# Optimization experiments

Measured on AMD Instinct MI355X. Metric: run time of the kernel, lower is better.

## Reference

```python
import jax, jax.numpy as jnp
import numpy as np

NUM_EMBEDDINGS = 1024
EMBEDDING_DIM = 128
COMMITMENT_COST = 1.0
DECAY = 0.99
EPSILON = 1e-05
N_TOKENS = 65536


def setup_inputs() -> dict:
    key = jax.random.key(0)
    k1, k2, k3 = jax.random.split(key, 3)
    inputs = jax.random.normal(k1, (N_TOKENS, EMBEDDING_DIM), dtype=jnp.float32)
    embedding = jax.random.normal(k2, (NUM_EMBEDDINGS, EMBEDDING_DIM), dtype=jnp.float32) * 0.01
    cluster_size = jnp.ones((NUM_EMBEDDINGS,), dtype=jnp.float32)
    embed_avg = jax.random.normal(k3, (NUM_EMBEDDINGS, EMBEDDING_DIM), dtype=jnp.float32) * 0.01
    return {"inputs": inputs, "embedding": embedding,
            "cluster_size": cluster_size, "embed_avg": embed_avg}


def reference(inputs, embedding, cluster_size, embed_avg):
    # inputs: [N, D], embedding: [K, D]
    flat = inputs.reshape(-1, EMBEDDING_DIM)
    distances = (jnp.sum(flat * flat, axis=1, keepdims=True)
                 + jnp.sum(embedding * embedding, axis=1)
                 - 2.0 * flat @ embedding.T)
    idx = jnp.argmin(distances, axis=1)                       # [N]
    quantized = embedding[idx].reshape(inputs.shape)          # direct gather (same math as one-hot matmul)

    # EMA update (training path); one-hot matmuls replaced by bincount/segment_sum
    dw = jnp.zeros((NUM_EMBEDDINGS,), dtype=flat.dtype).at[idx].add(1.0)   # encodings.sum(0)
    new_cluster_size = cluster_size * DECAY + (1.0 - DECAY) * dw
    dw_embed = jax.ops.segment_sum(flat, idx, num_segments=NUM_EMBEDDINGS)  # encodings.T @ flat
    new_embed_avg = embed_avg * DECAY + (1.0 - DECAY) * dw_embed
    n = jnp.sum(new_cluster_size)
    cs = (new_cluster_size + EPSILON) / (n + NUM_EMBEDDINGS * EPSILON) * n
    new_embedding = new_embed_avg / cs[:, None]

    # losses (quantized/inputs detach semantics are identical values in fwd)
    diff2 = jnp.mean((quantized - inputs) ** 2)
    loss = diff2 + COMMITMENT_COST * diff2

    # straight-through estimator: value equals quantized
    quantized_st = inputs + jax.lax.stop_gradient(quantized - inputs)
    return (quantized_st, loss, idx, new_embedding, new_cluster_size, new_embed_avg)
```

## Files before the change

kernel.cpp:

```cpp
#include <hip/hip_runtime.h>

typedef __attribute__((ext_vector_type(8))) _Float16 half8;
typedef __attribute__((ext_vector_type(4))) float f32x4;

constexpr int NTOK = 65536;
constexpr int DIM  = 128;
constexpr int NK   = 1024;

__global__ void bprep_k(const float* __restrict__ emb, char* __restrict__ bp,
                        float* __restrict__ embT, float* __restrict__ e2s,
                        double* __restrict__ en2d, int* __restrict__ nflag) {
  int i = blockIdx.x * 256 + threadIdx.x;
  if (i == 0) *nflag = 0;
  int c = i >> 4;
  int g = i & 15;
  float4 v0 = *(const float4*)&emb[c * 128 + g * 8];
  float4 v1 = *(const float4*)&emb[c * 128 + g * 8 + 4];
  float vf[8] = {v0.x, v0.y, v0.z, v0.w, v1.x, v1.y, v1.z, v1.w};
  half8 hv;
  double pacc = 0.0;
#pragma unroll
  for (int j = 0; j < 8; j++) {
    hv[j] = (_Float16)vf[j];
    embT[(g * 8 + j) * NK + c] = vf[j];
    pacc = fma((double)vf[j], (double)vf[j], pacc);
  }
  int chunk = c >> 5, n = (c >> 4) & 1, cl = c & 15;
  int kk = g >> 2, lo4 = g & 3;
  *(half8*)(bp + chunk * 8192 + kk * 2048 + n * 1024 + (lo4 * 16 + cl) * 16) = hv;
#pragma unroll
  for (int mask = 1; mask < 16; mask <<= 1) pacc += __shfl_xor(pacc, mask);
  if (g == 0) {
    en2d[c] = pacc;
    e2s[c] = (float)(pacc * 134217728.0 + 1073741824.0);
  }
}

__global__ __launch_bounds__(128, 2)
void argmin_k(const float* __restrict__ x, const char* __restrict__ bp,
              const float* __restrict__ e2s, int* __restrict__ idx_arr,
              float* __restrict__ out_idx, int* __restrict__ nflag,
              int* __restrict__ flags) {
  __shared__ unsigned kvs[2][64], k2s[2][64];
  const int t    = threadIdx.x;
  const int lane = t & 63;
  const int w    = t >> 6;
  const int l15  = lane & 15;
  const int lo4  = lane >> 4;
  const int rbase = blockIdx.x * 64;
  const int cbase = w * 16;
  const int lb16 = lane * 16;

  half8 FA[4][2], FB[4][2];

#define LOADG(DST, C, KK)                                                      \
  {                                                                            \
    const char* _b = bp + ((C) * 8192 + (KK) * 2048) + lb16;                   \
    DST[0] = *(const half8*)_b;                                                \
    DST[1] = *(const half8*)(_b + 1024);                                       \
  }

#pragma unroll
  for (int kk = 0; kk < 4; kk++) LOADG(FA[kk], cbase, kk)
#pragma unroll
  for (int kk = 0; kk < 4; kk++) LOADG(FB[kk], cbase + 1, kk)

  half8 ah[4][4];
#pragma unroll
  for (int m = 0; m < 4; m++)
#pragma unroll
    for (int kk = 0; kk < 4; kk++) {
      const float* xp = &x[(rbase + m * 16 + l15) * 128 + kk * 32 + lo4 * 8];
      float4 v0 = *(const float4*)xp;
      float4 v1 = *(const float4*)(xp + 4);
      float vf[8] = {v0.x, v0.y, v0.z, v0.w, v1.x, v1.y, v1.z, v1.w};
      half8 av;
#pragma unroll
      for (int j = 0; j < 8; j++) av[j] = (_Float16)vf[j];
      ah[m][kk] = av;
    }

  unsigned bv[4][4], b2[4][4];
#pragma unroll
  for (int m = 0; m < 4; m++)
#pragma unroll
    for (int r = 0; r < 4; r++) { bv[m][r] = 0xFFFFFFFFu; b2[m][r] = 0xFFFFFFFFu; }

#define MFMA_PHASE(BANK, KK)                                                   \
  {                                                                            \
    _Pragma("unroll")                                                          \
    for (int m = 0; m < 4; m++) {                                              \
      acc[m][0] = __builtin_amdgcn_mfma_f32_16x16x32_f16(ah[m][KK], BANK[KK][0], acc[m][0], 0, 0, 0); \
      acc[m][1] = __builtin_amdgcn_mfma_f32_16x16x32_f16(ah[m][KK], BANK[KK][1], acc[m][1], 0, 0, 0); \
    }                                                                          \
  }

#define KEY_EPI(C)                                                             \
  {                                                                            \
    _Pragma("unroll")                                                          \
    for (int n = 0; n < 2; n++) {                                              \
      unsigned col = (unsigned)((C) * 32 + n * 16 + l15);                      \
      float e2v = n ? e2b : e2a;                                               \
      _Pragma("unroll")                                                        \
      for (int m = 0; m < 4; m++)                                              \
        _Pragma("unroll")                                                      \
        for (int r = 0; r < 4; r++) {                                          \
          float ks = fmaf(acc[m][n][r], -268435456.0f, e2v);                   \
          unsigned key = ((unsigned)ks & 0xFFFFFC00u) | col;                   \
          unsigned old = bv[m][r];                                             \
          bv[m][r] = min(old, key);                                            \
          b2[m][r] = min(b2[m][r], max(old, key));                             \
        }                                                                      \
    }                                                                          \
  }

  for (int i = 0; i < 16; i += 2) {
    const int cg = cbase + i;
    {
      float e2a = e2s[cg * 32 + l15];
      float e2b = e2s[cg * 32 + 16 + l15];
      f32x4 acc[4][2];
#pragma unroll
      for (int m = 0; m < 4; m++)
#pragma unroll
        for (int n = 0; n < 2; n++) acc[m][n] = (f32x4)(0.0f);
#pragma unroll
      for (int kk = 0; kk < 4; kk++) {
        MFMA_PHASE(FA, kk)
        if (i + 2 < 16) LOADG(FA[kk], cg + 2, kk)
      }
      KEY_EPI(cg)
    }
    {
      float e2a = e2s[(cg + 1) * 32 + l15];
      float e2b = e2s[(cg + 1) * 32 + 16 + l15];
      f32x4 acc[4][2];
#pragma unroll
      for (int m = 0; m < 4; m++)
#pragma unroll
        for (int n = 0; n < 2; n++) acc[m][n] = (f32x4)(0.0f);
#pragma unroll
      for (int kk = 0; kk < 4; kk++) {
        MFMA_PHASE(FB, kk)
        if (i + 3 < 16) LOADG(FB[kk], cg + 3, kk)
      }
      KEY_EPI(cg + 1)
    }
  }
#undef LOADG
#undef MFMA_PHASE
#undef KEY_EPI

#pragma unroll
  for (int m = 0; m < 4; m++)
#pragma unroll
    for (int r = 0; r < 4; r++) {
      unsigned v = bv[m][r], v2 = b2[m][r];
      for (int mask = 1; mask < 16; mask <<= 1) {
        unsigned ov = __shfl_xor(v, mask);
        unsigned o2 = __shfl_xor(v2, mask);
        v2 = min(min(v2, o2), max(v, ov));
        v  = min(v, ov);
      }
      if (l15 == 0) {
        int lr = m * 16 + lo4 * 4 + r;
        kvs[w][lr] = v;
        k2s[w][lr] = v2;
      }
    }
  __syncthreads();

  if (t < 64) {
    unsigned va = kvs[0][t], vb = kvs[1][t];
    unsigned v2 = min(min(k2s[0][t], k2s[1][t]), max(va, vb));
    unsigned v  = min(va, vb);
    int row = rbase + t;
    int ii = (int)(v & 1023u);
    idx_arr[row] = ii;
    out_idx[row] = (float)ii;
    if ((v2 >> 10) - (v >> 10) < 79u) {
      int p = atomicAdd(nflag, 1); flags[p] = row;
    }
  }
}

__global__ __launch_bounds__(256)
void fb_k(const float* __restrict__ x, const float* __restrict__ embT,
          const double* __restrict__ en2d, const int* __restrict__ nflag,
          const int* __restrict__ flags, int* __restrict__ idx_arr,
          float* __restrict__ out_idx) {
  int n = *nflag;
  __shared__ double xsh[4][DIM];
  __shared__ double sv[256];
  __shared__ int    si[256];
  int t = threadIdx.x;
  double n0 = en2d[t * 4 + 0], n1 = en2d[t * 4 + 1];
  double n2 = en2d[t * 4 + 2], n3 = en2d[t * 4 + 3];
  for (int base = blockIdx.x * 4; base < n; base += gridDim.x * 4) {
    int nb = min(4, n - base);
    __syncthreads();
    for (int u = t; u < nb * DIM; u += 256) {
      int j = u >> 7, d = u & 127;
      xsh[j][d] = (double)x[flags[base + j] * DIM + d];
    }
    __syncthreads();
    double xe[4][4];
#pragma unroll
    for (int j = 0; j < 4; j++)
#pragma unroll
      for (int q = 0; q < 4; q++) xe[j][q] = 0.0;
    for (int d = 0; d < DIM; d++) {
      float4 v = *(const float4*)&embT[d * NK + t * 4];
      double e0 = (double)v.x, e1 = (double)v.y, e2 = (double)v.z, e3 = (double)v.w;
#pragma unroll
      for (int j = 0; j < 4; j++) {
        double xd = xsh[j][d];
        xe[j][0] = fma(e0, xd, xe[j][0]);
        xe[j][1] = fma(e1, xd, xe[j][1]);
        xe[j][2] = fma(e2, xd, xe[j][2]);
        xe[j][3] = fma(e3, xd, xe[j][3]);
      }
    }
#pragma unroll
    for (int j = 0; j < 4; j++) {
      double s0 = n0 - 2.0 * xe[j][0];
      double s1 = n1 - 2.0 * xe[j][1];
      double s2 = n2 - 2.0 * xe[j][2];
      double s3 = n3 - 2.0 * xe[j][3];
      double bvv = s0; int bii = t * 4;
      if (s1 < bvv) { bvv = s1; bii = t * 4 + 1; }
      if (s2 < bvv) { bvv = s2; bii = t * 4 + 2; }
      if (s3 < bvv) { bvv = s3; bii = t * 4 + 3; }
      sv[t] = bvv; si[t] = bii;
      __syncthreads();
      for (int sh = 128; sh > 0; sh >>= 1) {
        if (t < sh) {
          double ov = sv[t + sh]; int oi = si[t + sh];
          if (ov < sv[t] || (ov == sv[t] && oi < si[t])) { sv[t] = ov; si[t] = oi; }
        }
        __syncthreads();
      }
      if (t == 0 && j < nb) {
        int row = flags[base + j];
        idx_arr[row] = si[0];
        out_idx[row] = (float)si[0];
      }
      __syncthreads();
    }
  }
}

__global__ void histb_k(const int* __restrict__ idx, unsigned* __restrict__ bcount) {
  __shared__ unsigned bins[NK];
  int t = threadIdx.x;
  for (int b = t; b < NK; b += 256) bins[b] = 0u;
  __syncthreads();
#pragma unroll
  for (int j = 0; j < 4; j++)
    atomicAdd(&bins[idx[blockIdx.x * 1024 + j * 256 + t]], 1u);
  __syncthreads();
  for (int b = t; b < NK; b += 256) bcount[blockIdx.x * NK + b] = bins[b];
}

__global__ void scan_k(unsigned* __restrict__ bcount, unsigned* __restrict__ icounts,
                       unsigned* __restrict__ offsets, const float* __restrict__ cs,
                       float* __restrict__ out_ncs, float* __restrict__ csk) {
  __shared__ unsigned sc[NK];
  __shared__ float sf[NK];
  int t = threadIdx.x;
  unsigned tot = 0;
#pragma unroll 8
  for (int b = 0; b < 64; b++) tot += bcount[b * NK + t];
  icounts[t] = tot;
  sc[t] = tot;
  __syncthreads();
  for (int off = 1; off < NK; off <<= 1) {
    unsigned v = (t >= off) ? sc[t - off] : 0u;
    __syncthreads();
    sc[t] += v;
    __syncthreads();
  }
  unsigned excl = sc[t] - tot;
  offsets[t] = excl;
  unsigned run = excl;
#pragma unroll 8
  for (int b = 0; b < 64; b++) {
    unsigned c = bcount[b * NK + t];
    bcount[b * NK + t] = run;
    run += c;
  }
  float c0 = cs[t];
  float ncs = c0 * 0.99f + 0.01f * (float)tot;
  out_ncs[t] = ncs;
  sf[t] = c0;
  __syncthreads();
  for (int s = 512; s > 0; s >>= 1) {
    if (t < s) sf[t] += sf[t + s];
    __syncthreads();
  }
  float n = 0.99f * sf[0] + 655.36f;
  csk[t] = (ncs + 1e-5f) / (n + 1024.0f * 1e-5f) * n;
}

__global__ __launch_bounds__(1024)
void scatter_k(const int* __restrict__ idx, const unsigned* __restrict__ bstart,
               int* __restrict__ order) {
  __shared__ unsigned cur[NK];
  int t = threadIdx.x;
  cur[t] = bstart[blockIdx.x * NK + t];
  __syncthreads();
  int r = blockIdx.x * 1024 + t;
  unsigned p = atomicAdd(&cur[idx[r]], 1u);
  order[p] = r;
}

__global__ __launch_bounds__(512)
void fgather_k(const float* __restrict__ x, const float* __restrict__ emb,
               const unsigned* __restrict__ offsets, const unsigned* __restrict__ icounts,
               const int* __restrict__ order, float* __restrict__ out_q,
               float* __restrict__ dwsum4, float* __restrict__ partial4) {
  __shared__ int ids[1024];
  int k = blockIdx.x >> 2, q = blockIdx.x & 3;
  int t = threadIdx.x;
  int d = t & 127, h = t >> 7;
  unsigned cnt = icounts[k];
  unsigned qs = (cnt * (unsigned)q) >> 2;
  unsigned qe = (cnt * (unsigned)(q + 1)) >> 2;
  unsigned s = offsets[k] + qs;
  unsigned myc = qe - qs;
  for (unsigned j = t; j < myc && j < 1024u; j += 512) ids[j] = order[s + j];
  __syncthreads();
  float e = emb[k * DIM + d];
  float acc = 0.f, ls = 0.f;
#pragma unroll 2
  for (unsigned j = h; j < myc; j += 4) {
    int row = (j < 1024u) ? ids[j] : order[s + j];
    float xv = x[row * DIM + d];
    out_q[row * DIM + d] = e;
    acc += xv;
    float dd = e - xv;
    ls += dd * dd;
  }
  __shared__ float sa[512], sl[512];
  sa[t] = acc; sl[t] = ls;
  __syncthreads();
  if (t < 128) dwsum4[(q * NK + k) * DIM + t] = sa[t] + sa[t + 128] + sa[t + 256] + sa[t + 384];
  for (int sh = 256; sh > 0; sh >>= 1) {
    if (t < sh) sl[t] += sl[t + sh];
    __syncthreads();
  }
  if (t == 0) partial4[blockIdx.x] = sl[0];
}

__global__ void emb_k(const float* __restrict__ embed_avg, const float* __restrict__ dwsum4,
                      const float* __restrict__ csk, const float* __restrict__ partial4,
                      float* __restrict__ out_nemb, float* __restrict__ out_nea,
                      float* __restrict__ out_loss) {
  if (blockIdx.x == 0) {
    __shared__ float red[256];
    int t = threadIdx.x;
    float v = 0.f;
#pragma unroll
    for (int i = 0; i < 16; i++) v += partial4[t + 256 * i];
    red[t] = v;
    __syncthreads();
    for (int sh = 128; sh > 0; sh >>= 1) {
      if (t < sh) red[t] += red[t + sh];
      __syncthreads();
    }
    if (t == 0) out_loss[0] = 2.0f * red[0] / 8388608.0f;
    return;
  }
  int i = (blockIdx.x - 1) * 256 + threadIdx.x;
  float dw = dwsum4[i] + dwsum4[NK * DIM + i] + dwsum4[2 * NK * DIM + i] + dwsum4[3 * NK * DIM + i];
  float na = embed_avg[i] * 0.99f + 0.01f * dw;
  out_nea[i] = na;
  out_nemb[i] = na / csk[i >> 7];
}

extern "C" void kernel_launch(void* const* d_in, const int* in_sizes, int n_in,
                              void* d_out, int out_size, void* d_ws, size_t ws_size,
                              hipStream_t stream) {
  const float* x   = (const float*)d_in[0];
  const float* emb = (const float*)d_in[1];
  const float* cs  = (const float*)d_in[2];
  const float* ea  = (const float*)d_in[3];

  float* out      = (float*)d_out;
  float* out_q    = out;
  float* out_loss = out + 8388608;
  float* out_idx  = out + 8388609;
  float* out_nemb = out + 8454145;
  float* out_ncs  = out + 8585217;
  float* out_nea  = out + 8586241;

  float* W        = (float*)d_ws;
  float* e2s      = W;
  double* en2d    = (double*)(W + 1024);
  char*  bpack    = (char*)(W + 3072);
  float* embT     = W + 72704;
  unsigned* bcount = (unsigned*)(W + 203776);
  unsigned* icounts = (unsigned*)(W + 269312);
  unsigned* offsets = (unsigned*)(W + 270336);
  float* csk      = W + 271360;
  int*   nflag    = (int*)(W + 272384);
  int*   flags    = (int*)(W + 272400);
  int*   idx_arr  = (int*)(W + 337936);
  int*   order    = (int*)(W + 403472);
  float* dwsum4   = W + 469008;
  float* partial4 = W + 993296;

  bprep_k<<<64, 256, 0, stream>>>(emb, bpack, embT, e2s, en2d, nflag);
  argmin_k<<<1024, 128, 0, stream>>>(x, bpack, e2s, idx_arr, out_idx, nflag, flags);
  fb_k<<<256, 256, 0, stream>>>(x, embT, en2d, nflag, flags, idx_arr, out_idx);
  histb_k<<<64, 256, 0, stream>>>(idx_arr, bcount);
  scan_k<<<1, 1024, 0, stream>>>(bcount, icounts, offsets, cs, out_ncs, csk);
  scatter_k<<<64, 1024, 0, stream>>>(idx_arr, bcount, order);
  fgather_k<<<4096, 512, 0, stream>>>(x, emb, offsets, icounts, order, out_q, dwsum4, partial4);
  emb_k<<<513, 256, 0, stream>>>(ea, dwsum4, csk, partial4, out_nemb, out_nea, out_loss);
}
```

Measured before the change: 99.97 us.

## Fold histogram into argmin via global atomics and drop per-block bucket scan

Per-code counts are now accumulated with global atomics directly in the argmin kernel, and the fallback kernel adjusts them when it changes an index. The separate histogram kernel and the 64-way per-block count scan go away. The scatter then uses global atomic cursors in place of per-block shared cursors. This saves a kernel launch and the bcount traffic, at the cost of contended global atomics and a nondeterministic order within each bucket.

```diff
diff --git a/kernel.cpp b/kernel.cpp
--- a/kernel.cpp
+++ b/kernel.cpp
@@ -9,9 +9,11 @@
 
 __global__ void bprep_k(const float* __restrict__ emb, char* __restrict__ bp,
                         float* __restrict__ embT, float* __restrict__ e2s,
-                        double* __restrict__ en2d, int* __restrict__ nflag) {
+                        double* __restrict__ en2d, int* __restrict__ nflag,
+                        unsigned* __restrict__ icounts) {
   int i = blockIdx.x * 256 + threadIdx.x;
   if (i == 0) *nflag = 0;
+  if (i < NK) icounts[i] = 0u;
   int c = i >> 4;
   int g = i & 15;
   float4 v0 = *(const float4*)&emb[c * 128 + g * 8];
@@ -40,7 +42,7 @@
 void argmin_k(const float* __restrict__ x, const char* __restrict__ bp,
               const float* __restrict__ e2s, int* __restrict__ idx_arr,
               float* __restrict__ out_idx, int* __restrict__ nflag,
-              int* __restrict__ flags) {
+              int* __restrict__ flags, unsigned* __restrict__ icounts) {
   __shared__ unsigned kvs[2][64], k2s[2][64];
   const int t    = threadIdx.x;
   const int lane = t & 63;
@@ -178,6 +180,7 @@
     int ii = (int)(v & 1023u);
     idx_arr[row] = ii;
     out_idx[row] = (float)ii;
+    atomicAdd(&icounts[ii], 1u);
     if ((v2 >> 10) - (v >> 10) < 79u) {
       int p = atomicAdd(nflag, 1); flags[p] = row;
     }
@@ -188,7 +191,7 @@
 void fb_k(const float* __restrict__ x, const float* __restrict__ embT,
           const double* __restrict__ en2d, const int* __restrict__ nflag,
           const int* __restrict__ flags, int* __restrict__ idx_arr,
-          float* __restrict__ out_idx) {
+          float* __restrict__ out_idx, unsigned* __restrict__ icounts) {
   int n = *nflag;
   __shared__ double xsh[4][DIM];
   __shared__ double sv[256];
@@ -242,36 +245,27 @@
       }
       if (t == 0 && j < nb) {
         int row = flags[base + j];
-        idx_arr[row] = si[0];
-        out_idx[row] = (float)si[0];
+        int nw = si[0];
+        int old = idx_arr[row];
+        if (nw != old) {
+          idx_arr[row] = nw;
+          out_idx[row] = (float)nw;
+          atomicSub(&icounts[old], 1u);
+          atomicAdd(&icounts[nw], 1u);
+        }
       }
       __syncthreads();
     }
   }
 }
 
-__global__ void histb_k(const int* __restrict__ idx, unsigned* __restrict__ bcount) {
-  __shared__ unsigned bins[NK];
-  int t = threadIdx.x;
-  for (int b = t; b < NK; b += 256) bins[b] = 0u;
-  __syncthreads();
-#pragma unroll
-  for (int j = 0; j < 4; j++)
-    atomicAdd(&bins[idx[blockIdx.x * 1024 + j * 256 + t]], 1u);
-  __syncthreads();
-  for (int b = t; b < NK; b += 256) bcount[blockIdx.x * NK + b] = bins[b];
-}
-
-__global__ void scan_k(unsigned* __restrict__ bcount, unsigned* __restrict__ icounts,
-                       unsigned* __restrict__ offsets, const float* __restrict__ cs,
+__global__ void scan_k(const unsigned* __restrict__ icounts, unsigned* __restrict__ offsets,
+                       unsigned* __restrict__ cursors, const float* __restrict__ cs,
                        float* __restrict__ out_ncs, float* __restrict__ csk) {
   __shared__ unsigned sc[NK];
   __shared__ float sf[NK];
   int t = threadIdx.x;
-  unsigned tot = 0;
-#pragma unroll 8
-  for (int b = 0; b < 64; b++) tot += bcount[b * NK + t];
-  icounts[t] = tot;
+  unsigned tot = icounts[t];
   sc[t] = tot;
   __syncthreads();
   for (int off = 1; off < NK; off <<= 1) {
@@ -282,13 +276,7 @@
   }
   unsigned excl = sc[t] - tot;
   offsets[t] = excl;
-  unsigned run = excl;
-#pragma unroll 8
-  for (int b = 0; b < 64; b++) {
-    unsigned c = bcount[b * NK + t];
-    bcount[b * NK + t] = run;
-    run += c;
-  }
+  cursors[t] = excl;
   float c0 = cs[t];
   float ncs = c0 * 0.99f + 0.01f * (float)tot;
   out_ncs[t] = ncs;
@@ -303,14 +291,11 @@
 }
 
 __global__ __launch_bounds__(1024)
-void scatter_k(const int* __restrict__ idx, const unsigned* __restrict__ bstart,
+void scatter_k(const int* __restrict__ idx, unsigned* __restrict__ cursors,
                int* __restrict__ order) {
-  __shared__ unsigned cur[NK];
-  int t = threadIdx.x;
-  cur[t] = bstart[blockIdx.x * NK + t];
-  __syncthreads();
-  int r = blockIdx.x * 1024 + t;
-  unsigned p = atomicAdd(&cur[idx[r]], 1u);
+  int r = blockIdx.x * 1024 + threadIdx.x;
+  int k = idx[r];
+  unsigned p = atomicAdd(&cursors[k], 1u);
   order[p] = r;
 }
 
@@ -399,23 +384,22 @@
   double* en2d    = (double*)(W + 1024);
   char*  bpack    = (char*)(W + 3072);
   float* embT     = W + 72704;
-  unsigned* bcount = (unsigned*)(W + 203776);
-  unsigned* icounts = (unsigned*)(W + 269312);
-  unsigned* offsets = (unsigned*)(W + 270336);
-  float* csk      = W + 271360;
-  int*   nflag    = (int*)(W + 272384);
-  int*   flags    = (int*)(W + 272400);
-  int*   idx_arr  = (int*)(W + 337936);
-  int*   order    = (int*)(W + 403472);
-  float* dwsum4   = W + 469008;
-  float* partial4 = W + 993296;
-
-  bprep_k<<<64, 256, 0, stream>>>(emb, bpack, embT, e2s, en2d, nflag);
-  argmin_k<<<1024, 128, 0, stream>>>(x, bpack, e2s, idx_arr, out_idx, nflag, flags);
-  fb_k<<<256, 256, 0, stream>>>(x, embT, en2d, nflag, flags, idx_arr, out_idx);
-  histb_k<<<64, 256, 0, stream>>>(idx_arr, bcount);
-  scan_k<<<1, 1024, 0, stream>>>(bcount, icounts, offsets, cs, out_ncs, csk);
-  scatter_k<<<64, 1024, 0, stream>>>(idx_arr, bcount, order);
+  unsigned* icounts = (unsigned*)(W + 203776);
+  unsigned* offsets = (unsigned*)(W + 204800);
+  unsigned* cursors = (unsigned*)(W + 205824);
+  float* csk      = W + 206848;
+  int*   nflag    = (int*)(W + 207872);
+  int*   flags    = (int*)(W + 207888);
+  int*   idx_arr  = (int*)(W + 273424);
+  int*   order    = (int*)(W + 338960);
+  float* dwsum4   = W + 404496;
+  float* partial4 = W + 928784;
+
+  bprep_k<<<64, 256, 0, stream>>>(emb, bpack, embT, e2s, en2d, nflag, icounts);
+  argmin_k<<<1024, 128, 0, stream>>>(x, bpack, e2s, idx_arr, out_idx, nflag, flags, icounts);
+  fb_k<<<256, 256, 0, stream>>>(x, embT, en2d, nflag, flags, idx_arr, out_idx, icounts);
+  scan_k<<<1, 1024, 0, stream>>>(icounts, offsets, cursors, cs, out_ncs, csk);
+  scatter_k<<<64, 1024, 0, stream>>>(idx_arr, cursors, order);
   fgather_k<<<4096, 512, 0, stream>>>(x, emb, offsets, icounts, order, out_q, dwsum4, partial4);
   emb_k<<<513, 256, 0, stream>>>(ea, dwsum4, csk, partial4, out_nemb, out_nea, out_loss);
 }
```

Result: slower. 112.4 us (+12.4%).
